# Kernel tuning notes

Hardware: AMD Instinct MI355X
Metric: run time of the kernel (lower is better)

## Reference

```python
import jax, jax.numpy as jnp
import numpy as np

B, S, E, H = 4, 4096, 1024, 128

def setup_inputs() -> dict:
    key = jax.random.key(0)
    kx, kk, kq, kv = jax.random.split(key, 4)
    x = jax.random.normal(kx, (B, S, E), dtype=jnp.float32)
    # torch nn.Linear weights are [out_features, in_features]
    Wk = jax.random.normal(kk, (H, E), dtype=jnp.float32) * (E ** -0.5)
    Wq = jax.random.normal(kq, (H, E), dtype=jnp.float32) * (E ** -0.5)
    Wv = jax.random.normal(kv, (H, E), dtype=jnp.float32) * (E ** -0.5)
    return {"x": x, "Wk": Wk, "Wq": Wq, "Wv": Wv}

def reference(x, Wk, Wq, Wv):
    # projections: y = x @ W.T  (bias-free nn.Linear)
    k = jnp.einsum('bse,he->bsh', x, Wk)
    q = jnp.einsum('bse,he->bsh', x, Wq)
    v = jnp.einsum('bse,he->bsh', x, Wv)
    emb = x.shape[-1]
    # scores scaled by embedding_size**-0.5 (as in the source, not head_size)
    scores = jnp.einsum('bqh,bkh->bqk', q, k) * (emb ** -0.5)  # [B,S,S]
    # causal mask: positions j > i get -inf
    i = jnp.arange(scores.shape[-2])[:, None]
    j = jnp.arange(scores.shape[-1])[None, :]
    scores = jnp.where(j > i, jnp.float32(-jnp.inf), scores)
    probs = jax.nn.softmax(scores, axis=-1)
    # dropout is identity in eval mode
    out = jnp.einsum('bqk,bkh->bqh', probs, v)  # [B,S,H]
    return out
```

## Files before the change

kernel.cpp:

```cpp
#include <hip/hip_runtime.h>

typedef short bf16x8 __attribute__((ext_vector_type(8)));
typedef float f32x4 __attribute__((ext_vector_type(4)));

#define MFMA16(a, b, c) __builtin_amdgcn_mfma_f32_16x16x32_bf16(a, b, c, 0, 0, 0)

constexpr int Bn = 4, Sn = 4096, En = 1024, Hn = 128;
constexpr float CSCALE = 1.44269504089f * 0.03125f;

__device__ inline unsigned short f2bf(float f) {
    unsigned int u = __builtin_bit_cast(unsigned int, f);
    u += 0x7fff + ((u >> 16) & 1);
    return (unsigned short)(u >> 16);
}

__device__ inline unsigned int pk2(float a, float b) {
    unsigned int ua = __builtin_bit_cast(unsigned int, a) + 0x8000u;
    unsigned int ub = __builtin_bit_cast(unsigned int, b) + 0x8000u;
    return __builtin_amdgcn_perm(ub, ua, 0x07060302u);
}

__device__ inline void gld16(const unsigned short* g, unsigned short* l) {
    __builtin_amdgcn_global_load_lds((const __attribute__((address_space(1))) void*)g,
                                     (__attribute__((address_space(3))) void*)l, 16, 0, 0);
}

__global__ __launch_bounds__(256, 2) void proj_kernel(
    const float* __restrict__ x,
    const float* __restrict__ Wk, const float* __restrict__ Wq, const float* __restrict__ Wv,
    unsigned short* __restrict__ qb, unsigned short* __restrict__ kb,
    unsigned short* __restrict__ vbT)
{
    __shared__ unsigned short xs[64][68];
    __shared__ unsigned short wsm[128][68];

    const int gy = blockIdx.y;
    const float* W = (gy == 0) ? Wq : (gy == 1) ? Wk : Wv;

    const int m0 = blockIdx.x * 64;
    const int tid = threadIdx.x;
    const int lane = tid & 63, wave = tid >> 6;
    const int l15 = lane & 15, quad = lane >> 4;
    const int wm = (wave & 1) * 32;
    const int wn = (wave >> 1) * 64;

    f32x4 acc[2][4] = {};

    float4 xp[4], wp[8];
    for (int p = 0; p < 4; ++p) {
        int i = p * 256 + tid, row = i >> 4, c = (i & 15) * 4;
        xp[p] = *(const float4*)&x[(size_t)(m0 + row) * En + c];
    }
    for (int p = 0; p < 8; ++p) {
        int i = p * 256 + tid, row = i >> 4, c = (i & 15) * 4;
        wp[p] = *(const float4*)&W[(size_t)row * En + c];
    }

    for (int kc = 0; kc < En / 64; ++kc) {
        for (int p = 0; p < 4; ++p) {
            int i = p * 256 + tid, row = i >> 4, c = (i & 15) * 4;
            uint2 w2 = { pk2(xp[p].x, xp[p].y), pk2(xp[p].z, xp[p].w) };
            *(uint2*)&xs[row][c] = w2;
        }
        for (int p = 0; p < 8; ++p) {
            int i = p * 256 + tid, row = i >> 4, c = (i & 15) * 4;
            uint2 w2 = { pk2(wp[p].x, wp[p].y), pk2(wp[p].z, wp[p].w) };
            *(uint2*)&wsm[row][c] = w2;
        }
        __syncthreads();
        if (kc + 1 < En / 64) {
            int k0 = (kc + 1) * 64;
            for (int p = 0; p < 4; ++p) {
                int i = p * 256 + tid, row = i >> 4, c = (i & 15) * 4;
                xp[p] = *(const float4*)&x[(size_t)(m0 + row) * En + k0 + c];
            }
            for (int p = 0; p < 8; ++p) {
                int i = p * 256 + tid, row = i >> 4, c = (i & 15) * 4;
                wp[p] = *(const float4*)&W[(size_t)row * En + k0 + c];
            }
        }
        if (gy != 2) {
            for (int kk = 0; kk < 2; ++kk) {
                bf16x8 af[2], bfr[4];
                for (int i = 0; i < 2; ++i) af[i]  = *(const bf16x8*)&xs[wm + i * 16 + l15][kk * 32 + quad * 8];
                for (int j = 0; j < 4; ++j) bfr[j] = *(const bf16x8*)&wsm[wn + j * 16 + l15][kk * 32 + quad * 8];
                for (int i = 0; i < 2; ++i)
                    for (int j = 0; j < 4; ++j)
                        acc[i][j] = MFMA16(af[i], bfr[j], acc[i][j]);
            }
        } else {
            for (int kk = 0; kk < 2; ++kk) {
                bf16x8 aw[4], bx[2];
                for (int j = 0; j < 4; ++j) aw[j] = *(const bf16x8*)&wsm[wn + j * 16 + l15][kk * 32 + quad * 8];
                for (int i = 0; i < 2; ++i) bx[i] = *(const bf16x8*)&xs[wm + i * 16 + l15][kk * 32 + quad * 8];
                for (int i = 0; i < 2; ++i)
                    for (int j = 0; j < 4; ++j)
                        acc[i][j] = MFMA16(aw[j], bx[i], acc[i][j]);
            }
        }
        __syncthreads();
    }

    if (gy != 2) {
        unsigned short* ob = (gy == 0) ? qb : kb;
        const float osc = (gy == 0) ? CSCALE : 1.0f;
        for (int i = 0; i < 2; ++i) {
            int rowb = m0 + wm + i * 16 + quad * 4;
            for (int j = 0; j < 4; ++j) {
                int col = wn + j * 16 + l15;
                for (int r = 0; r < 4; ++r)
                    ob[(size_t)(rowb + r) * Hn + col] = f2bf(acc[i][j][r] * osc);
            }
        }
    } else {
        for (int j = 0; j < 4; ++j) {
            int hb = wn + j * 16 + quad * 4;
            for (int i = 0; i < 2; ++i) {
                int sp = m0 + wm + i * 16 + l15;
                int bb = sp >> 12, ss = sp & 4095;
                for (int r = 0; r < 4; ++r)
                    vbT[((size_t)(bb * 128 + hb + r)) * Sn + ss] = f2bf(acc[i][j][r]);
            }
        }
    }
}

__global__ __launch_bounds__(256, 2) void attn_kernel(
    const unsigned short* __restrict__ qb, const unsigned short* __restrict__ kb,
    const unsigned short* __restrict__ vbT, float* __restrict__ out)
{
    __shared__ __align__(16) unsigned char smem[70144];
    unsigned short* psb = (unsigned short*)(smem + 65536);

    const int b = blockIdx.y;
    const int qt = (int)gridDim.x - 1 - (int)blockIdx.x;
    const int q0 = qt * 32;
    const int tid = threadIdx.x;
    const int lane = tid & 63, wave = tid >> 6;
    const int l15 = lane & 15, quad = lane >> 4;
    const int g = wave & 1;
    const int p = wave >> 1;

    const unsigned short* qg = qb + (size_t)(b * Sn + q0) * Hn;
    bf16x8 qf[4];
    {
        int qrow = g * 16 + l15;
        for (int f = 0; f < 4; ++f)
            qf[f] = *(const bf16x8*)&qg[qrow * Hn + f * 32 + quad * 8];
    }

    f32x4 o[8] = {};
    float m_r = -INFINITY, l_r = 0.f;

    const int nkt = qt + 1;
    const int ni = (nkt + 1) >> 1;

    const unsigned short* kg = kb + (size_t)b * Sn * Hn;
    const unsigned short* vg = vbT + (size_t)b * 128 * Sn;

    unsigned short* psrow = &psb[(p * 32 + g * 16 + l15) * 36];

    auto issue = [&](int kt, int c) {
        char* base = (char*)smem + (p * 2 + c) * 16384;
        int kt0 = kt * 32;
        for (int j = 0; j < 4; ++j) {
            int seg = (g * 4 + j) * 1024;
            int dk = seg + lane * 16;
            int key = dk >> 8, ch = (dk >> 4) & 15;
            gld16(kg + (size_t)(kt0 + key) * Hn + ((ch ^ (key & 7)) << 3),
                  (unsigned short*)(base + seg));
            int h = dk >> 6, cc = (dk >> 4) & 3;
            gld16(vg + (size_t)h * Sn + kt0 + ((cc ^ (h & 3)) << 3),
                  (unsigned short*)(base + 8192 + seg));
        }
    };

    if (p < nkt) issue(p, 0);

    for (int it = 0; it < ni; ++it) {
        const int kt = 2 * it + p;
        __syncthreads();
        if (kt + 2 < nkt) issue(kt + 2, (it + 1) & 1);
        if (kt < nkt) {
            unsigned short* kbase = (unsigned short*)((char*)smem + (p * 2 + (it & 1)) * 16384);
            unsigned short* vbase = kbase + 4096;

            float u[2][4];
            for (int nt = 0; nt < 2; ++nt) {
                f32x4 s = {};
                for (int kk = 0; kk < 4; ++kk) {
                    int ch = (kk * 4 + quad) ^ (l15 & 7);
                    bf16x8 kf = *(const bf16x8*)&kbase[(nt * 16 + l15) * 128 + ch * 8];
                    s = MFMA16(kf, qf[kk], s);
                }
                for (int r = 0; r < 4; ++r) u[nt][r] = s[r];
            }
            if (kt == nkt - 1) {
                int qq = g * 16 + l15;
                for (int nt = 0; nt < 2; ++nt)
                    for (int r = 0; r < 4; ++r)
                        if (nt * 16 + quad * 4 + r > qq) u[nt][r] = -INFINITY;
            }
            float mx = -INFINITY;
            for (int nt = 0; nt < 2; ++nt)
                for (int r = 0; r < 4; ++r) mx = fmaxf(mx, u[nt][r]);
            mx = fmaxf(mx, __shfl_xor(mx, 16));
            mx = fmaxf(mx, __shfl_xor(mx, 32));
            float mn = fmaxf(m_r, mx);
            float alpha = exp2f(m_r - mn);
            m_r = mn;
            float sum = 0.f;
            for (int nt = 0; nt < 2; ++nt)
                for (int r = 0; r < 4; ++r) {
                    float pv = exp2f(u[nt][r] - mn);
                    u[nt][r] = pv;
                    sum += pv;
                }
            sum += __shfl_xor(sum, 16);
            sum += __shfl_xor(sum, 32);
            l_r = l_r * alpha + sum;

            for (int nt = 0; nt < 2; ++nt) {
                uint2 w2 = { pk2(u[nt][0], u[nt][1]), pk2(u[nt][2], u[nt][3]) };
                *(uint2*)&psrow[nt * 16 + quad * 4] = w2;
            }
            for (int t = 0; t < 8; ++t) o[t] *= alpha;

            bf16x8 pf = *(const bf16x8*)&psrow[quad * 8];
            for (int t = 0; t < 8; ++t) {
                int hh = t * 16 + l15;
                bf16x8 vf = *(const bf16x8*)&vbase[hh * 32 + ((quad ^ (l15 & 3)) << 3)];
                o[t] = MFMA16(vf, pf, o[t]);
            }
        }
    }
    __syncthreads();

    float* mo = (float*)smem;
    float* ml = (float*)(smem + 20480);
    if (p == 1) {
        for (int t = 0; t < 8; ++t)
            for (int r = 0; r < 4; ++r)
                mo[(size_t)(g * 128 + t * 16 + quad * 4 + r) * 17 + l15] = o[t][r];
        if (quad == 0) {
            ml[g * 32 + l15] = m_r;
            ml[g * 32 + 16 + l15] = l_r;
        }
    }
    __syncthreads();
    if (p == 0) {
        float m1 = ml[g * 32 + l15];
        float l1 = ml[g * 32 + 16 + l15];
        float M = fmaxf(m_r, m1);
        float w0 = exp2f(m_r - M);
        float w1 = exp2f(m1 - M);
        float L = w0 * l_r + w1 * l1;
        float inv = 1.0f / L;
        float* og = out + (size_t)(b * Sn + q0 + g * 16 + l15) * Hn;
        for (int t = 0; t < 8; ++t) {
            float4 st;
            float* mor = &mo[(size_t)(g * 128 + t * 16 + quad * 4) * 17 + l15];
            st.x = (w0 * o[t][0] + w1 * mor[0 * 17]) * inv;
            st.y = (w0 * o[t][1] + w1 * mor[1 * 17]) * inv;
            st.z = (w0 * o[t][2] + w1 * mor[2 * 17]) * inv;
            st.w = (w0 * o[t][3] + w1 * mor[3 * 17]) * inv;
            *(float4*)&og[t * 16 + quad * 4] = st;
        }
    }
}

extern "C" void kernel_launch(void* const* d_in, const int* in_sizes, int n_in,
                              void* d_out, int out_size, void* d_ws, size_t ws_size,
                              hipStream_t stream)
{
    const float* x  = (const float*)d_in[0];
    const float* Wk = (const float*)d_in[1];
    const float* Wq = (const float*)d_in[2];
    const float* Wv = (const float*)d_in[3];
    float* out = (float*)d_out;

    unsigned short* qbuf  = (unsigned short*)d_ws;
    unsigned short* kbuf  = qbuf + (size_t)Bn * Sn * Hn;
    unsigned short* vbufT = kbuf + (size_t)Bn * Sn * Hn;

    proj_kernel<<<dim3(Bn * Sn / 64, 3), 256, 0, stream>>>(x, Wk, Wq, Wv, qbuf, kbuf, vbufT);
    attn_kernel<<<dim3(Sn / 32, Bn), 256, 0, stream>>>(qbuf, kbuf, vbufT, out);
}
```

Before: 213.5 us.

## Split attention KV into chunks with merge kernel; pre-convert weights and double-buffer projection

Attention is split across up to four KV chunks of 32 tiles per query tile (split-K / flash-decoding style). Partial outputs plus max and sum are written to a workspace and combined by a new merge kernel, which evens out the causal load imbalance. K/V fragments are now loaded straight from global memory into registers with register double-buffering, so LDS staging and per-iteration barriers are gone. A prep kernel converts the weights to bf16 once, and the projection kernel now double-buffers LDS, fetches W with async global-to-LDS loads using XOR swizzling, and targets occupancy 3. In exchange it adds two extra launches, partial-result traffic and higher register pressure.

```diff
diff --git a/kernel.cpp b/kernel.cpp
--- a/kernel.cpp
+++ b/kernel.cpp
@@ -25,17 +25,39 @@
                                      (__attribute__((address_space(3))) void*)l, 16, 0, 0);
 }
 
-__global__ __launch_bounds__(256, 2) void proj_kernel(
-    const float* __restrict__ x,
+__device__ inline int slot_base(int qt) {
+    int a = qt >> 5, r = qt & 31;
+    return qt + 16 * a * (a - 1) + r * a;
+}
+constexpr int SLOTS_PER_B = 320;
+constexpr int SLOT_F = 4160;
+
+__global__ __launch_bounds__(256) void prep_kernel(
     const float* __restrict__ Wk, const float* __restrict__ Wq, const float* __restrict__ Wv,
+    unsigned short* __restrict__ wb)
+{
+    int gy = blockIdx.x >> 5;
+    const float* src = (gy == 0) ? Wq : (gy == 1) ? Wk : Wv;
+    unsigned short* dst = wb + (size_t)gy * Hn * En;
+    int t = (blockIdx.x & 31) * 256 + threadIdx.x;
+    const float4* s4 = (const float4*)src;
+    for (int i = 0; i < 4; ++i) {
+        float4 v = s4[(size_t)t * 4 + i];
+        uint2 w2 = { pk2(v.x, v.y), pk2(v.z, v.w) };
+        *(uint2*)&dst[(size_t)t * 16 + i * 4] = w2;
+    }
+}
+
+__global__ __launch_bounds__(256, 3) void proj_kernel(
+    const float* __restrict__ x, const unsigned short* __restrict__ wb,
     unsigned short* __restrict__ qb, unsigned short* __restrict__ kb,
     unsigned short* __restrict__ vbT)
 {
-    __shared__ unsigned short xs[64][68];
-    __shared__ unsigned short wsm[128][68];
+    __shared__ __align__(16) unsigned short xs[2][64][64];
+    __shared__ __align__(16) unsigned short wsm[2][128][64];
 
     const int gy = blockIdx.y;
-    const float* W = (gy == 0) ? Wq : (gy == 1) ? Wk : Wv;
+    const unsigned short* wg = wb + (size_t)gy * Hn * En;
 
     const int m0 = blockIdx.x * 64;
     const int tid = threadIdx.x;
@@ -45,60 +67,69 @@
     const int wn = (wave >> 1) * 64;
 
     f32x4 acc[2][4] = {};
-
-    float4 xp[4], wp[8];
-    for (int p = 0; p < 4; ++p) {
-        int i = p * 256 + tid, row = i >> 4, c = (i & 15) * 4;
-        xp[p] = *(const float4*)&x[(size_t)(m0 + row) * En + c];
-    }
-    for (int p = 0; p < 8; ++p) {
-        int i = p * 256 + tid, row = i >> 4, c = (i & 15) * 4;
-        wp[p] = *(const float4*)&W[(size_t)row * En + c];
-    }
+    float4 xp[4];
+
+    auto loadx = [&](int kc) {
+        for (int p4 = 0; p4 < 4; ++p4) {
+            int i = p4 * 256 + tid, row = i >> 4, c4 = (i & 15) * 4;
+            xp[p4] = *(const float4*)&x[(size_t)(m0 + row) * En + kc * 64 + c4];
+        }
+    };
+    auto writex = [&](int c) {
+        for (int p4 = 0; p4 < 4; ++p4) {
+            int i = p4 * 256 + tid, row = i >> 4, hc = i & 15;
+            uint2 w2 = { pk2(xp[p4].x, xp[p4].y), pk2(xp[p4].z, xp[p4].w) };
+            *(uint2*)((char*)&xs[c][0][0] + row * 128 + (((hc >> 1) ^ (row & 7)) << 4) + ((hc & 1) << 3)) = w2;
+        }
+    };
+    auto issueW = [&](int kc, int c) {
+        for (int j = 0; j < 4; ++j) {
+            int seg = (wave * 4 + j) * 1024;
+            int d = seg + (lane << 4);
+            int row = d >> 7, chp = (d >> 4) & 7;
+            gld16(wg + (size_t)row * En + kc * 64 + ((chp ^ (row & 7)) << 3),
+                  (unsigned short*)((char*)&wsm[c][0][0] + seg));
+        }
+    };
+
+    loadx(0);
+    issueW(0, 0);
+    writex(0);
+    loadx(1);
 
     for (int kc = 0; kc < En / 64; ++kc) {
-        for (int p = 0; p < 4; ++p) {
-            int i = p * 256 + tid, row = i >> 4, c = (i & 15) * 4;
-            uint2 w2 = { pk2(xp[p].x, xp[p].y), pk2(xp[p].z, xp[p].w) };
-            *(uint2*)&xs[row][c] = w2;
-        }
-        for (int p = 0; p < 8; ++p) {
-            int i = p * 256 + tid, row = i >> 4, c = (i & 15) * 4;
-            uint2 w2 = { pk2(wp[p].x, wp[p].y), pk2(wp[p].z, wp[p].w) };
-            *(uint2*)&wsm[row][c] = w2;
-        }
+        const int c = kc & 1;
         __syncthreads();
         if (kc + 1 < En / 64) {
-            int k0 = (kc + 1) * 64;
-            for (int p = 0; p < 4; ++p) {
-                int i = p * 256 + tid, row = i >> 4, c = (i & 15) * 4;
-                xp[p] = *(const float4*)&x[(size_t)(m0 + row) * En + k0 + c];
-            }
-            for (int p = 0; p < 8; ++p) {
-                int i = p * 256 + tid, row = i >> 4, c = (i & 15) * 4;
-                wp[p] = *(const float4*)&W[(size_t)row * En + k0 + c];
-            }
-        }
+            issueW(kc + 1, c ^ 1);
+            writex(c ^ 1);
+            int kn = (kc + 2 < En / 64) ? kc + 2 : En / 64 - 1;
+            loadx(kn);
+        }
+        bf16x8 xf[2][2], wf[4][2];
+        for (int i = 0; i < 2; ++i)
+            for (int kk = 0; kk < 2; ++kk) {
+                int row = wm + i * 16 + l15;
+                int chn = (kk * 4 + quad) ^ (row & 7);
+                xf[i][kk] = *(const bf16x8*)((char*)&xs[c][0][0] + row * 128 + (chn << 4));
+            }
+        for (int j = 0; j < 4; ++j)
+            for (int kk = 0; kk < 2; ++kk) {
+                int row = wn + j * 16 + l15;
+                int chn = (kk * 4 + quad) ^ (row & 7);
+                wf[j][kk] = *(const bf16x8*)((char*)&wsm[c][0][0] + row * 128 + (chn << 4));
+            }
         if (gy != 2) {
-            for (int kk = 0; kk < 2; ++kk) {
-                bf16x8 af[2], bfr[4];
-                for (int i = 0; i < 2; ++i) af[i]  = *(const bf16x8*)&xs[wm + i * 16 + l15][kk * 32 + quad * 8];
-                for (int j = 0; j < 4; ++j) bfr[j] = *(const bf16x8*)&wsm[wn + j * 16 + l15][kk * 32 + quad * 8];
+            for (int kk = 0; kk < 2; ++kk)
                 for (int i = 0; i < 2; ++i)
                     for (int j = 0; j < 4; ++j)
-                        acc[i][j] = MFMA16(af[i], bfr[j], acc[i][j]);
-            }
+                        acc[i][j] = MFMA16(xf[i][kk], wf[j][kk], acc[i][j]);
         } else {
-            for (int kk = 0; kk < 2; ++kk) {
-                bf16x8 aw[4], bx[2];
-                for (int j = 0; j < 4; ++j) aw[j] = *(const bf16x8*)&wsm[wn + j * 16 + l15][kk * 32 + quad * 8];
-                for (int i = 0; i < 2; ++i) bx[i] = *(const bf16x8*)&xs[wm + i * 16 + l15][kk * 32 + quad * 8];
+            for (int kk = 0; kk < 2; ++kk)
                 for (int i = 0; i < 2; ++i)
                     for (int j = 0; j < 4; ++j)
-                        acc[i][j] = MFMA16(aw[j], bx[i], acc[i][j]);
-            }
-        }
-        __syncthreads();
+                        acc[i][j] = MFMA16(wf[j][kk], xf[i][kk], acc[i][j]);
+        }
     }
 
     if (gy != 2) {
@@ -125,16 +156,25 @@
     }
 }
 
-__global__ __launch_bounds__(256, 2) void attn_kernel(
+__global__ __launch_bounds__(256, 3) void attn_kernel(
     const unsigned short* __restrict__ qb, const unsigned short* __restrict__ kb,
-    const unsigned short* __restrict__ vbT, float* __restrict__ out)
-{
-    __shared__ __align__(16) unsigned char smem[70144];
-    unsigned short* psb = (unsigned short*)(smem + 65536);
-
-    const int b = blockIdx.y;
-    const int qt = (int)gridDim.x - 1 - (int)blockIdx.x;
+    const unsigned short* __restrict__ vbT, float* __restrict__ out,
+    float* __restrict__ part)
+{
+    __shared__ unsigned short ps[4][16][36];
+    __shared__ float mo[2][128][17];
+    __shared__ float ml[2][2][16];
+
+    const int qt = blockIdx.x;
+    const int ch = blockIdx.y;
+    const int b  = blockIdx.z;
+    const int nkt = qt + 1;
+    const int nch = (nkt + 31) >> 5;
+    if (ch >= nch) return;
+    const int c0 = ch * 32;
+    const int nloc = min(32, nkt - c0);
     const int q0 = qt * 32;
+
     const int tid = threadIdx.x;
     const int lane = tid & 63, wave = tid >> 6;
     const int l15 = lane & 15, quad = lane >> 4;
@@ -143,129 +183,160 @@
 
     const unsigned short* qg = qb + (size_t)(b * Sn + q0) * Hn;
     bf16x8 qf[4];
-    {
-        int qrow = g * 16 + l15;
-        for (int f = 0; f < 4; ++f)
-            qf[f] = *(const bf16x8*)&qg[qrow * Hn + f * 32 + quad * 8];
-    }
+    for (int f = 0; f < 4; ++f)
+        qf[f] = *(const bf16x8*)&qg[(g * 16 + l15) * Hn + f * 32 + quad * 8];
 
     f32x4 o[8] = {};
     float m_r = -INFINITY, l_r = 0.f;
 
-    const int nkt = qt + 1;
-    const int ni = (nkt + 1) >> 1;
-
-    const unsigned short* kg = kb + (size_t)b * Sn * Hn;
-    const unsigned short* vg = vbT + (size_t)b * 128 * Sn;
-
-    unsigned short* psrow = &psb[(p * 32 + g * 16 + l15) * 36];
-
-    auto issue = [&](int kt, int c) {
-        char* base = (char*)smem + (p * 2 + c) * 16384;
-        int kt0 = kt * 32;
-        for (int j = 0; j < 4; ++j) {
-            int seg = (g * 4 + j) * 1024;
-            int dk = seg + lane * 16;
-            int key = dk >> 8, ch = (dk >> 4) & 15;
-            gld16(kg + (size_t)(kt0 + key) * Hn + ((ch ^ (key & 7)) << 3),
-                  (unsigned short*)(base + seg));
-            int h = dk >> 6, cc = (dk >> 4) & 3;
-            gld16(vg + (size_t)h * Sn + kt0 + ((cc ^ (h & 3)) << 3),
-                  (unsigned short*)(base + 8192 + seg));
-        }
+    const unsigned short* kA = kb + (size_t)b * Sn * Hn + l15 * 128 + quad * 8;
+    const unsigned short* vA = vbT + (size_t)b * 128 * Sn + (size_t)l15 * 4096 + quad * 8;
+    unsigned short* psrow = &ps[wave][l15][0];
+
+    bf16x8 kf[2][8], vf[2][8];
+    auto loadKV = [&](int gt, int buf) {
+        for (int nt = 0; nt < 2; ++nt)
+            for (int kk = 0; kk < 4; ++kk)
+                kf[buf][nt * 4 + kk] = *(const bf16x8*)(kA + (size_t)gt * 4096 + nt * 2048 + kk * 32);
+        for (int t = 0; t < 8; ++t)
+            vf[buf][t] = *(const bf16x8*)(vA + (size_t)t * 65536 + gt * 32);
     };
 
-    if (p < nkt) issue(p, 0);
-
-    for (int it = 0; it < ni; ++it) {
-        const int kt = 2 * it + p;
-        __syncthreads();
-        if (kt + 2 < nkt) issue(kt + 2, (it + 1) & 1);
-        if (kt < nkt) {
-            unsigned short* kbase = (unsigned short*)((char*)smem + (p * 2 + (it & 1)) * 16384);
-            unsigned short* vbase = kbase + 4096;
-
-            float u[2][4];
-            for (int nt = 0; nt < 2; ++nt) {
-                f32x4 s = {};
-                for (int kk = 0; kk < 4; ++kk) {
-                    int ch = (kk * 4 + quad) ^ (l15 & 7);
-                    bf16x8 kf = *(const bf16x8*)&kbase[(nt * 16 + l15) * 128 + ch * 8];
-                    s = MFMA16(kf, qf[kk], s);
-                }
-                for (int r = 0; r < 4; ++r) u[nt][r] = s[r];
-            }
-            if (kt == nkt - 1) {
-                int qq = g * 16 + l15;
-                for (int nt = 0; nt < 2; ++nt)
-                    for (int r = 0; r < 4; ++r)
-                        if (nt * 16 + quad * 4 + r > qq) u[nt][r] = -INFINITY;
-            }
-            float mx = -INFINITY;
+    if (p < nloc) loadKV(c0 + p, 0);
+    int buf = 0;
+    for (int t_loc = p; t_loc < nloc; t_loc += 2, buf ^= 1) {
+        if (t_loc + 2 < nloc) loadKV(c0 + t_loc + 2, buf ^ 1);
+        const int gt = c0 + t_loc;
+
+        float u[2][4];
+        for (int nt = 0; nt < 2; ++nt) {
+            f32x4 s = {};
+            for (int kk = 0; kk < 4; ++kk) s = MFMA16(kf[buf][nt * 4 + kk], qf[kk], s);
+            for (int r = 0; r < 4; ++r) u[nt][r] = s[r];
+        }
+        if (gt == qt) {
+            int qq = g * 16 + l15;
             for (int nt = 0; nt < 2; ++nt)
-                for (int r = 0; r < 4; ++r) mx = fmaxf(mx, u[nt][r]);
-            mx = fmaxf(mx, __shfl_xor(mx, 16));
-            mx = fmaxf(mx, __shfl_xor(mx, 32));
-            float mn = fmaxf(m_r, mx);
-            float alpha = exp2f(m_r - mn);
-            m_r = mn;
-            float sum = 0.f;
-            for (int nt = 0; nt < 2; ++nt)
-                for (int r = 0; r < 4; ++r) {
-                    float pv = exp2f(u[nt][r] - mn);
-                    u[nt][r] = pv;
-                    sum += pv;
-                }
-            sum += __shfl_xor(sum, 16);
-            sum += __shfl_xor(sum, 32);
-            l_r = l_r * alpha + sum;
-
-            for (int nt = 0; nt < 2; ++nt) {
-                uint2 w2 = { pk2(u[nt][0], u[nt][1]), pk2(u[nt][2], u[nt][3]) };
-                *(uint2*)&psrow[nt * 16 + quad * 4] = w2;
-            }
-            for (int t = 0; t < 8; ++t) o[t] *= alpha;
-
-            bf16x8 pf = *(const bf16x8*)&psrow[quad * 8];
-            for (int t = 0; t < 8; ++t) {
-                int hh = t * 16 + l15;
-                bf16x8 vf = *(const bf16x8*)&vbase[hh * 32 + ((quad ^ (l15 & 3)) << 3)];
-                o[t] = MFMA16(vf, pf, o[t]);
-            }
-        }
-    }
+                for (int r = 0; r < 4; ++r)
+                    if (nt * 16 + quad * 4 + r > qq) u[nt][r] = -INFINITY;
+        }
+        float mx = -INFINITY;
+        for (int nt = 0; nt < 2; ++nt)
+            for (int r = 0; r < 4; ++r) mx = fmaxf(mx, u[nt][r]);
+        mx = fmaxf(mx, __shfl_xor(mx, 16));
+        mx = fmaxf(mx, __shfl_xor(mx, 32));
+        float mn = fmaxf(m_r, mx);
+        float alpha = exp2f(m_r - mn);
+        m_r = mn;
+        float sum = 0.f;
+        for (int nt = 0; nt < 2; ++nt)
+            for (int r = 0; r < 4; ++r) {
+                float pv = exp2f(u[nt][r] - mn);
+                u[nt][r] = pv;
+                sum += pv;
+            }
+        sum += __shfl_xor(sum, 16);
+        sum += __shfl_xor(sum, 32);
+        l_r = l_r * alpha + sum;
+
+        for (int nt = 0; nt < 2; ++nt) {
+            uint2 w2 = { pk2(u[nt][0], u[nt][1]), pk2(u[nt][2], u[nt][3]) };
+            *(uint2*)&psrow[nt * 16 + quad * 4] = w2;
+        }
+        for (int t = 0; t < 8; ++t) o[t] *= alpha;
+
+        bf16x8 pf = *(const bf16x8*)&psrow[quad * 8];
+        for (int t = 0; t < 8; ++t)
+            o[t] = MFMA16(vf[buf][t], pf, o[t]);
+    }
+
     __syncthreads();
-
-    float* mo = (float*)smem;
-    float* ml = (float*)(smem + 20480);
     if (p == 1) {
         for (int t = 0; t < 8; ++t)
             for (int r = 0; r < 4; ++r)
-                mo[(size_t)(g * 128 + t * 16 + quad * 4 + r) * 17 + l15] = o[t][r];
+                mo[g][t * 16 + quad * 4 + r][l15] = o[t][r];
         if (quad == 0) {
-            ml[g * 32 + l15] = m_r;
-            ml[g * 32 + 16 + l15] = l_r;
+            ml[g][0][l15] = m_r;
+            ml[g][1][l15] = l_r;
         }
     }
     __syncthreads();
     if (p == 0) {
-        float m1 = ml[g * 32 + l15];
-        float l1 = ml[g * 32 + 16 + l15];
+        float m1 = ml[g][0][l15];
+        float l1 = ml[g][1][l15];
         float M = fmaxf(m_r, m1);
         float w0 = exp2f(m_r - M);
         float w1 = exp2f(m1 - M);
         float L = w0 * l_r + w1 * l1;
-        float inv = 1.0f / L;
-        float* og = out + (size_t)(b * Sn + q0 + g * 16 + l15) * Hn;
-        for (int t = 0; t < 8; ++t) {
-            float4 st;
-            float* mor = &mo[(size_t)(g * 128 + t * 16 + quad * 4) * 17 + l15];
-            st.x = (w0 * o[t][0] + w1 * mor[0 * 17]) * inv;
-            st.y = (w0 * o[t][1] + w1 * mor[1 * 17]) * inv;
-            st.z = (w0 * o[t][2] + w1 * mor[2 * 17]) * inv;
-            st.w = (w0 * o[t][3] + w1 * mor[3 * 17]) * inv;
-            *(float4*)&og[t * 16 + quad * 4] = st;
-        }
+        if (nch == 1) {
+            float inv = 1.0f / L;
+            float* og = out + (size_t)(b * Sn + q0 + g * 16 + l15) * Hn;
+            for (int t = 0; t < 8; ++t) {
+                float4 st;
+                st.x = (w0 * o[t][0] + w1 * mo[g][t * 16 + quad * 4 + 0][l15]) * inv;
+                st.y = (w0 * o[t][1] + w1 * mo[g][t * 16 + quad * 4 + 1][l15]) * inv;
+                st.z = (w0 * o[t][2] + w1 * mo[g][t * 16 + quad * 4 + 2][l15]) * inv;
+                st.w = (w0 * o[t][3] + w1 * mo[g][t * 16 + quad * 4 + 3][l15]) * inv;
+                *(float4*)&og[t * 16 + quad * 4] = st;
+            }
+        } else {
+            float* P = part + (size_t)(b * SLOTS_PER_B + slot_base(qt) + ch) * SLOT_F;
+            int q = g * 16 + l15;
+            for (int t = 0; t < 8; ++t) {
+                float4 st;
+                st.x = w0 * o[t][0] + w1 * mo[g][t * 16 + quad * 4 + 0][l15];
+                st.y = w0 * o[t][1] + w1 * mo[g][t * 16 + quad * 4 + 1][l15];
+                st.z = w0 * o[t][2] + w1 * mo[g][t * 16 + quad * 4 + 2][l15];
+                st.w = w0 * o[t][3] + w1 * mo[g][t * 16 + quad * 4 + 3][l15];
+                *(float4*)&P[q * 128 + t * 16 + quad * 4] = st;
+            }
+            if (quad == 0) {
+                P[4096 + q] = M;
+                P[4128 + q] = L;
+            }
+        }
+    }
+}
+
+__global__ __launch_bounds__(256) void merge_kernel(
+    const float* __restrict__ part, float* __restrict__ out)
+{
+    const int qt = 32 + blockIdx.x;
+    const int b = blockIdx.y;
+    const int nch = (qt >> 5) + 1;
+    const float* P0 = part + (size_t)(b * SLOTS_PER_B + slot_base(qt)) * SLOT_F;
+    const int q = threadIdx.x >> 3;
+    const int h0 = (threadIdx.x & 7) * 16;
+
+    float m[4], w[4];
+    float M = -INFINITY;
+    for (int c = 0; c < nch; ++c) {
+        m[c] = P0[(size_t)c * SLOT_F + 4096 + q];
+        M = fmaxf(M, m[c]);
+    }
+    float L = 0.f;
+    for (int c = 0; c < nch; ++c) {
+        w[c] = exp2f(m[c] - M);
+        L += w[c] * P0[(size_t)c * SLOT_F + 4128 + q];
+    }
+    float inv = 1.0f / L;
+
+    float acc[16] = {};
+    for (int c = 0; c < nch; ++c) {
+        const float* Pq = P0 + (size_t)c * SLOT_F + q * 128 + h0;
+        for (int j = 0; j < 4; ++j) {
+            float4 v = *(const float4*)&Pq[j * 4];
+            acc[j * 4 + 0] += w[c] * v.x;
+            acc[j * 4 + 1] += w[c] * v.y;
+            acc[j * 4 + 2] += w[c] * v.z;
+            acc[j * 4 + 3] += w[c] * v.w;
+        }
+    }
+    float* og = out + (size_t)(b * Sn + qt * 32 + q) * Hn + h0;
+    for (int j = 0; j < 4; ++j) {
+        float4 st = { acc[j * 4 + 0] * inv, acc[j * 4 + 1] * inv,
+                      acc[j * 4 + 2] * inv, acc[j * 4 + 3] * inv };
+        *(float4*)&og[j * 4] = st;
     }
 }
 
@@ -282,7 +353,11 @@
     unsigned short* qbuf  = (unsigned short*)d_ws;
     unsigned short* kbuf  = qbuf + (size_t)Bn * Sn * Hn;
     unsigned short* vbufT = kbuf + (size_t)Bn * Sn * Hn;
-
-    proj_kernel<<<dim3(Bn * Sn / 64, 3), 256, 0, stream>>>(x, Wk, Wq, Wv, qbuf, kbuf, vbufT);
-    attn_kernel<<<dim3(Sn / 32, Bn), 256, 0, stream>>>(qbuf, kbuf, vbufT, out);
-}
+    unsigned short* wb    = vbufT + (size_t)Bn * Sn * Hn;
+    float* part = (float*)(wb + (size_t)3 * Hn * En);
+
+    prep_kernel<<<96, 256, 0, stream>>>(Wk, Wq, Wv, wb);
+    proj_kernel<<<dim3(Bn * Sn / 64, 3), 256, 0, stream>>>(x, wb, qbuf, kbuf, vbufT);
+    attn_kernel<<<dim3(128, 4, Bn), 256, 0, stream>>>(qbuf, kbuf, vbufT, out, part);
+    merge_kernel<<<dim3(96, Bn), 256, 0, stream>>>(part, out);
+}
```

Result: slower. 590.6 us (+176.7%).
